# Kernel tuning notes

Measured on AMD Instinct MI355X. Metric: run time of the kernel, lower is better.

The kernel has to match this reference:

```python
import jax, jax.numpy as jnp
import numpy as np

B, N, CT, CS, CP, H, NB = 1, 1024, 768, 384, 16, 16, 4
DH = CT // H
NL, NK = 8, 32          # n_local_tokens, n_keys
K = NL + NK
SCALE = 1.0 / np.sqrt(DH)


def _ln(x, g=None, b=None, eps=1e-5):
    m = jnp.mean(x, -1, keepdims=True)
    v = jnp.var(x, -1, keepdims=True)
    y = (x - m) * jax.lax.rsqrt(v + eps)
    if g is not None:
        y = y * g
    if b is not None:
        y = y + b
    return y


def _adaln(a, s, sln_g, sw, sb, shw):
    # AF3 AdaLN: a <- sigmoid(Lin(s_n)) * LN(a) + LinNoBias(s_n)
    an = _ln(a)
    sn = _ln(s, sln_g)
    return jax.nn.sigmoid(sn @ sw + sb) * an + sn @ shw


def _indices(X_L):
    # n_local sequence neighbours (clamped window) + n_keys spatial nearest
    off = jnp.arange(NL) - NL // 2
    loc = jnp.clip(jnp.arange(N)[:, None] + off[None, :], 0, N - 1)  # [N,NL]
    d2 = jnp.sum((X_L[:, :, None, :] - X_L[:, None, :, :]) ** 2, -1)  # [B,N,N]
    _, nk = jax.lax.top_k(-d2, NK)                                    # [B,N,NK]
    loc = jnp.broadcast_to(loc[None], (X_L.shape[0], N, NL))
    return jnp.concatenate([loc, nk], -1)                             # [B,N,K]


def setup_inputs() -> dict:
    key = jax.random.key(0)
    ks = list(jax.random.split(key, 24))
    f32 = jnp.float32

    def rn(k, shape, s=0.02):
        return (jax.random.normal(k, shape) * s).astype(f32)

    d = {}
    d['A_I'] = jax.random.normal(ks[0], (B, N, CT), f32)
    d['S_I'] = jax.random.normal(ks[1], (B, N, CS), f32)
    d['Z_II'] = jax.random.normal(ks[2], (B, N, N, CP), f32)
    d['X_L'] = jax.random.normal(ks[3], (B, N, 3), f32) * 10.0
    d['f'] = jax.random.randint(ks[4], (B, N), 0, 4)
    # attention-pair-bias block params (stacked over NB blocks)
    d['aln1_sln_g'] = jnp.ones((NB, CS), f32)
    d['aln1_sw'] = rn(ks[5], (NB, CS, CT))
    d['aln1_sb'] = jnp.zeros((NB, CT), f32)
    d['aln1_shw'] = rn(ks[6], (NB, CS, CT))
    d['Wq'] = rn(ks[7], (NB, CT, CT))
    d['bq'] = jnp.zeros((NB, CT), f32)
    d['Wk'] = rn(ks[8], (NB, CT, CT))
    d['Wv'] = rn(ks[9], (NB, CT, CT))
    d['pair_ln_g'] = jnp.ones((NB, CP), f32)
    d['pair_ln_b'] = jnp.zeros((NB, CP), f32)
    d['Wb'] = rn(ks[10], (NB, CP, H))
    d['Wg'] = rn(ks[11], (NB, CT, CT))
    d['Wo'] = rn(ks[12], (NB, CT, CT))
    d['sg_w'] = rn(ks[13], (NB, CS, CT))
    d['sg_b'] = jnp.full((NB, CT), -2.0, f32)   # LinearBiasInit(-2.0)
    # conditioned transition block params
    d['aln2_sln_g'] = jnp.ones((NB, CS), f32)
    d['aln2_sw'] = rn(ks[14], (NB, CS, CT))
    d['aln2_sb'] = jnp.zeros((NB, CT), f32)
    d['aln2_shw'] = rn(ks[15], (NB, CS, CT))
    d['t_w1'] = rn(ks[16], (NB, CT, 2 * CT))
    d['t_w2'] = rn(ks[17], (NB, CT, 2 * CT))
    d['t_w3'] = rn(ks[18], (NB, 2 * CT, CT))
    d['tsg_w'] = rn(ks[19], (NB, CS, CT))
    d['tsg_b'] = jnp.full((NB, CT), -2.0, f32)
    return d


def reference(A_I, S_I, Z_II, X_L, f,
              aln1_sln_g, aln1_sw, aln1_sb, aln1_shw,
              Wq, bq, Wk, Wv, pair_ln_g, pair_ln_b, Wb, Wg, Wo, sg_w, sg_b,
              aln2_sln_g, aln2_sw, aln2_sb, aln2_shw,
              t_w1, t_w2, t_w3, tsg_w, tsg_b):
    idx = _indices(X_L)                       # [B,N,K] int
    bb = jnp.arange(B)[:, None, None]
    nn_ = jnp.arange(N)[None, :, None]
    zg = Z_II[bb, nn_, idx]                   # [B,N,K,CP] gathered pair reps
    A = A_I
    for i in range(NB):
        # LocalAttentionPairBias
        an = _adaln(A, S_I, aln1_sln_g[i], aln1_sw[i], aln1_sb[i], aln1_shw[i])
        q = (an @ Wq[i] + bq[i]).reshape(B, N, H, DH)
        kg = (an @ Wk[i])[bb, idx].reshape(B, N, K, H, DH)
        vg = (an @ Wv[i])[bb, idx].reshape(B, N, K, H, DH)
        bias = _ln(zg, pair_ln_g[i], pair_ln_b[i]) @ Wb[i]      # [B,N,K,H]
        sc = jnp.einsum('bnhd,bnkhd->bnhk', q, kg) * SCALE + jnp.swapaxes(bias, -1, -2)
        w = jax.nn.softmax(sc, -1)                               # [B,N,H,K]
        o = jnp.einsum('bnhk,bnkhd->bnhd', w, vg).reshape(B, N, CT)
        o = jax.nn.sigmoid(an @ Wg[i]) * o                       # per-channel gate
        o = jax.nn.sigmoid(S_I @ sg_w[i] + sg_b[i]) * (o @ Wo[i])
        A = A + o                                                # dropout=0 (eval)
        # ConditionedTransitionBlock (SwiGLU, n=2)
        an2 = _adaln(A, S_I, aln2_sln_g[i], aln2_sw[i], aln2_sb[i], aln2_shw[i])
        hb = jax.nn.silu(an2 @ t_w1[i]) * (an2 @ t_w2[i])
        A = A + jax.nn.sigmoid(S_I @ tsg_w[i] + tsg_b[i]) * (hb @ t_w3[i])
    return A
```

## Files before the change

kernel.cpp:

```cpp
#include <hip/hip_runtime.h>
#include <hip/hip_bf16.h>
#include <math.h>
#include <stdint.h>

#define NTOK 1024
#define CT   768
#define CS   384
#define CP   16
#define NH   16
#define DH   48
#define NBLK 4
#define NL   8
#define NKEY 32
#define KTOT 40
#define SCALE_ 0.14433756729740643f

#define WS_BLK      8257536
#define OFF_A1SW    0
#define OFF_A1SHW   294912
#define OFF_QKVG    589824
#define OFF_WO      2949120
#define OFF_SGT     3538944
#define OFF_A2SW    4128768
#define OFF_A2SHW   4423680
#define OFF_TW1     4718592
#define OFF_TW2     5898240
#define OFF_TW3     7077888

typedef __attribute__((ext_vector_type(8))) short short8;
typedef __attribute__((ext_vector_type(4))) float f32x4;

#define AS1 __attribute__((address_space(1)))
#define AS3 __attribute__((address_space(3)))

__device__ __forceinline__ float sigmoidf_(float x) {
    return 1.0f / (1.0f + __expf(-x));
}
__device__ __forceinline__ float bf2f(unsigned short u) {
    union { unsigned int i; float f; } v; v.i = (unsigned int)u << 16; return v.f;
}

__device__ __forceinline__ void gl_lds16(const void* g, void* l) {
    __builtin_amdgcn_global_load_lds((const AS1 void*)(uintptr_t)g,
                                     (AS3 void*)(uintptr_t)l, 16, 0, 0);
}

__global__ __launch_bounds__(256)
void topk_kernel(const float* __restrict__ X, int* __restrict__ idx) {
    const int w = threadIdx.x >> 6;
    const int l = threadIdx.x & 63;
    const int n = blockIdx.x * 4 + w;

    const float x0 = X[n * 3 + 0], x1 = X[n * 3 + 1], x2 = X[n * 3 + 2];
    float d[16];
    unsigned long long lkey = ~0ull;
#pragma unroll
    for (int j = 0; j < 16; ++j) {
        int m = j * 64 + l;
        float dx = x0 - X[m * 3 + 0];
        float dy = x1 - X[m * 3 + 1];
        float dz = x2 - X[m * 3 + 2];
        float v = dx * dx + dy * dy + dz * dz;
        d[j] = v;
        unsigned long long key =
            ((unsigned long long)__float_as_uint(v) << 32) | (unsigned int)m;
        lkey = key < lkey ? key : lkey;
    }
    if (l < NL) {
        int loc = n + l - NL / 2;
        loc = loc < 0 ? 0 : (loc > NTOK - 1 ? NTOK - 1 : loc);
        idx[n * KTOT + l] = loc;
    }

    for (int it = 0; it < NKEY; ++it) {
        unsigned long long rk = lkey;
#pragma unroll
        for (int s = 32; s > 0; s >>= 1) {
            unsigned long long o = __shfl_xor(rk, s, 64);
            rk = o < rk ? o : rk;
        }
        unsigned int win = (unsigned int)rk;
        if (l == 0) idx[n * KTOT + NL + it] = (int)win;
        if ((int)(win & 63) == l) {
            int jw = (int)(win >> 6);
            unsigned long long nk = ~0ull;
#pragma unroll
            for (int j = 0; j < 16; ++j) {
                if (j == jw) d[j] = INFINITY;
                unsigned long long key =
                    ((unsigned long long)__float_as_uint(d[j]) << 32) |
                    (unsigned int)(j * 64 + l);
                nk = key < nk ? key : nk;
            }
            lkey = nk;
        }
    }
}

__global__ __launch_bounds__(384)
void sprep_kernel(const float* __restrict__ S, const float* __restrict__ g1,
                  const float* __restrict__ g2,
                  __hip_bfloat16* __restrict__ S_bf,
                  __hip_bfloat16* __restrict__ snb) {
    int r = blockIdx.x, t = threadIdx.x;
    int wid = t >> 6, l = t & 63;
    __shared__ float ls[12];
    float v = S[r * CS + t];
    float s = v;
#pragma unroll
    for (int m = 32; m > 0; m >>= 1) s += __shfl_xor(s, m, 64);
    if (l == 0) ls[wid] = s;
    __syncthreads();
    float mean = (ls[0] + ls[1] + ls[2] + ls[3] + ls[4] + ls[5]) * (1.0f / CS);
    float d = v - mean;
    float q = d * d;
#pragma unroll
    for (int m = 32; m > 0; m >>= 1) q += __shfl_xor(q, m, 64);
    if (l == 0) ls[6 + wid] = q;
    __syncthreads();
    float rstd = rsqrtf((ls[6] + ls[7] + ls[8] + ls[9] + ls[10] + ls[11]) *
                        (1.0f / CS) + 1e-5f);
    float ln = d * rstd;
    S_bf[r * CS + t] = __float2bfloat16(v);
#pragma unroll
    for (int j = 0; j < 8; ++j) {
        const float* g = ((j & 1) ? g2 : g1) + (j >> 1) * CS;
        snb[((size_t)j * NTOK + r) * CS + t] = __float2bfloat16(ln * g[t]);
    }
}

__global__ __launch_bounds__(256)
void adaapply_kernel(const float* __restrict__ A,
                     const __hip_bfloat16* __restrict__ SIG,
                     const __hip_bfloat16* __restrict__ SH,
                     __hip_bfloat16* __restrict__ an) {
    int r = blockIdx.x, t = threadIdx.x;
    int wid = t >> 6, l = t & 63;
    __shared__ float ls[8];
    const float* ar = A + (size_t)r * CT;
    float v0 = ar[t], v1 = ar[t + 256], v2 = ar[t + 512];
    float s = v0 + v1 + v2;
#pragma unroll
    for (int m = 32; m > 0; m >>= 1) s += __shfl_xor(s, m, 64);
    if (l == 0) ls[wid] = s;
    __syncthreads();
    float mean = (ls[0] + ls[1] + ls[2] + ls[3]) * (1.0f / CT);
    float d0 = v0 - mean, d1 = v1 - mean, d2 = v2 - mean;
    float q = d0 * d0 + d1 * d1 + d2 * d2;
#pragma unroll
    for (int m = 32; m > 0; m >>= 1) q += __shfl_xor(q, m, 64);
    if (l == 0) ls[4 + wid] = q;
    __syncthreads();
    float rstd = rsqrtf((ls[4] + ls[5] + ls[6] + ls[7]) * (1.0f / CT) + 1e-5f);
    size_t base = (size_t)r * CT;
    float dd[3] = {d0, d1, d2};
#pragma unroll
    for (int k = 0; k < 3; ++k) {
        int c = t + k * 256;
        float sg = sigmoidf_(__bfloat162float(SIG[base + c]));
        float sh = __bfloat162float(SH[base + c]);
        an[base + c] = __float2bfloat16(sg * dd[k] * rstd + sh);
    }
}

struct ConvDesc { const float* src; __hip_bfloat16* dst; int K; int N; int tstart; int srcStride; };
struct ConvTable { ConvDesc e[14]; };

__global__ __launch_bounds__(256)
void convT_kernel(ConvTable tab) {
    int b = blockIdx.x;
    int ei = 0;
#pragma unroll
    for (int j = 1; j < 14; ++j) if (b >= tab.e[j].tstart) ei = j;
    ConvDesc d = tab.e[ei];
    const float* src = d.src + (size_t)blockIdx.y * d.srcStride;
    __hip_bfloat16* dst = d.dst + (size_t)blockIdx.y * WS_BLK;
    int tt = b - d.tstart;
    int ntn = d.N / 32;
    int k0 = (tt / ntn) * 32, n0 = (tt % ntn) * 32;
    __shared__ float s[32][33];
    int tx = threadIdx.x & 31, ty = threadIdx.x >> 5;
#pragma unroll
    for (int i = 0; i < 4; ++i)
        s[ty + 8 * i][tx] = src[(size_t)(k0 + ty + 8 * i) * d.N + n0 + tx];
    __syncthreads();
#pragma unroll
    for (int i = 0; i < 4; ++i)
        dst[(size_t)(n0 + ty + 8 * i) * d.K + k0 + tx] = __float2bfloat16(s[tx][ty + 8 * i]);
}

__global__ __launch_bounds__(256)
void biasprep_kernel(const float* __restrict__ bq, const float* __restrict__ sg_b,
                     const float* __restrict__ tsg_b, float* __restrict__ qb,
                     float* __restrict__ sb2) {
    int t = blockIdx.x * 256 + threadIdx.x;
    if (t < NBLK * 3072) {
        int i = t / 3072, c = t % 3072;
        qb[t] = (c < 768) ? bq[i * 768 + c] : 0.0f;
    }
    if (t < NBLK * 1536) {
        int i = t / 1536, c = t % 1536;
        sb2[t] = (c < 768) ? sg_b[i * 768 + c] : tsg_b[i * 768 + c - 768];
    }
}

template <int MODE>
__global__ __launch_bounds__(256)
void gemm_kernel(const __hip_bfloat16* __restrict__ A,
                 const __hip_bfloat16* B1,
                 const __hip_bfloat16* B2,
                 const float* __restrict__ cb1,
                 const float* __restrict__ cb2,
                 const __hip_bfloat16* __restrict__ auxb, int ld_aux,
                 float* __restrict__ outf,
                 __hip_bfloat16* outb,
                 __hip_bfloat16* outb2,
                 int K, int N, int ldo) {
    constexpr bool DUAL = (MODE == 2 || MODE == 5);
    __shared__ __align__(16) char As[8192];
    __shared__ __align__(16) char Bs[8192];
    __shared__ __align__(16) char Bs2[DUAL ? 8192 : 16];

    const float* cb = cb1;
    if constexpr (MODE == 5) {
        size_t z = blockIdx.z;
        A += z * (size_t)(NTOK * CS);
        B1 += (z >> 1) * (size_t)WS_BLK + (z & 1) * (size_t)OFF_A2SW;
        B2 = B1 + OFF_A1SHW;
        cb = ((z & 1) ? cb2 : cb1) + (z >> 1) * CT;
        outb += z * (size_t)(NTOK * CT);
        outb2 += z * (size_t)(NTOK * CT);
    } else if constexpr (MODE == 6) {
        size_t z = blockIdx.z;
        B1 += z * (size_t)WS_BLK;
        cb = cb1 + z * 1536;
        outb += z * (size_t)(NTOK * 1536);
    }

    const int tid = threadIdx.x;
    const int lane = tid & 63;
    const int wid = tid >> 6;
    const int wr = wid >> 1, wc = wid & 1;
    const int row0 = blockIdx.y * 64;
    const int col0 = blockIdx.x * 64;

    const int srow = tid >> 3;
    const int sg_e = (((tid & 7) ^ (srow & 7)) << 3);
    const __hip_bfloat16* ag = A + (size_t)(row0 + srow) * K + sg_e;
    const __hip_bfloat16* bg = B1 + (size_t)(col0 + srow) * K + sg_e;
    const __hip_bfloat16* bg2 = DUAL ? (B2 + (size_t)(col0 + srow) * K + sg_e) : nullptr;
    const size_t r32K = (size_t)32 * K;
    char* alds = As + tid * 16;
    char* blds = Bs + tid * 16;
    char* blds2 = Bs2 + tid * 16;

    f32x4 acc[2][2];
    f32x4 acc2[2][2];
#pragma unroll
    for (int i = 0; i < 2; ++i)
#pragma unroll
        for (int j = 0; j < 2; ++j) {
            acc[i][j] = (f32x4){0.f, 0.f, 0.f, 0.f};
            acc2[i][j] = (f32x4){0.f, 0.f, 0.f, 0.f};
        }

    const int l15 = lane & 15;
    const int lhi = lane >> 4;

    for (int k0 = 0; k0 < K; k0 += 64) {
        gl_lds16(ag, alds); gl_lds16(ag + r32K, alds + 4096);
        gl_lds16(bg, blds); gl_lds16(bg + r32K, blds + 4096);
        if (DUAL) { gl_lds16(bg2, blds2); gl_lds16(bg2 + r32K, blds2 + 4096); }
        ag += 64; bg += 64; if (DUAL) bg2 += 64;
        __syncthreads();
#pragma unroll
        for (int kk = 0; kk < 2; ++kk) {
            const int c = lhi + 4 * kk;
            const int ra0 = wr * 32 + l15, ra1 = ra0 + 16;
            const int rb0 = wc * 32 + l15, rb1 = rb0 + 16;
            short8 a0 = *(const short8*)(As + ra0 * 128 + (((c ^ (ra0 & 7)) << 4)));
            short8 a1 = *(const short8*)(As + ra1 * 128 + (((c ^ (ra1 & 7)) << 4)));
            short8 b0 = *(const short8*)(Bs + rb0 * 128 + (((c ^ (rb0 & 7)) << 4)));
            short8 b1 = *(const short8*)(Bs + rb1 * 128 + (((c ^ (rb1 & 7)) << 4)));
            acc[0][0] = __builtin_amdgcn_mfma_f32_16x16x32_bf16(a0, b0, acc[0][0], 0, 0, 0);
            acc[0][1] = __builtin_amdgcn_mfma_f32_16x16x32_bf16(a0, b1, acc[0][1], 0, 0, 0);
            acc[1][0] = __builtin_amdgcn_mfma_f32_16x16x32_bf16(a1, b0, acc[1][0], 0, 0, 0);
            acc[1][1] = __builtin_amdgcn_mfma_f32_16x16x32_bf16(a1, b1, acc[1][1], 0, 0, 0);
            if (DUAL) {
                short8 c0 = *(const short8*)(Bs2 + rb0 * 128 + (((c ^ (rb0 & 7)) << 4)));
                short8 c1 = *(const short8*)(Bs2 + rb1 * 128 + (((c ^ (rb1 & 7)) << 4)));
                acc2[0][0] = __builtin_amdgcn_mfma_f32_16x16x32_bf16(a0, c0, acc2[0][0], 0, 0, 0);
                acc2[0][1] = __builtin_amdgcn_mfma_f32_16x16x32_bf16(a0, c1, acc2[0][1], 0, 0, 0);
                acc2[1][0] = __builtin_amdgcn_mfma_f32_16x16x32_bf16(a1, c0, acc2[1][0], 0, 0, 0);
                acc2[1][1] = __builtin_amdgcn_mfma_f32_16x16x32_bf16(a1, c1, acc2[1][1], 0, 0, 0);
            }
        }
        __syncthreads();
    }

#pragma unroll
    for (int mi = 0; mi < 2; ++mi)
#pragma unroll
        for (int ni = 0; ni < 2; ++ni) {
            f32x4 v1 = acc[mi][ni];
            f32x4 v2 = acc2[mi][ni];
            int col = col0 + wc * 32 + ni * 16 + l15;
            int rbase = row0 + wr * 32 + mi * 16 + lhi * 4;
#pragma unroll
            for (int r = 0; r < 4; ++r) {
                int row = rbase + r;
                size_t o = (size_t)row * ldo + col;
                if (MODE == 2) {
                    float x = v1[r];
                    outb[o] = __float2bfloat16(x * sigmoidf_(x) * v2[r]);
                } else if (MODE == 3) {
                    float g = sigmoidf_(__bfloat162float(auxb[(size_t)row * ld_aux + col]));
                    outf[o] += g * v1[r];
                } else if (MODE == 4 || MODE == 6) {
                    outb[o] = __float2bfloat16(v1[r] + cb[col]);
                } else {
                    outb[o] = __float2bfloat16(v1[r] + cb[col]);
                    outb2[o] = __float2bfloat16(v2[r]);
                }
            }
        }
}

__global__ __launch_bounds__(256)
void attn_kernel(const __hip_bfloat16* __restrict__ qkvg,
                 const float* __restrict__ Z,
                 const int* __restrict__ idx,
                 const float* __restrict__ pg, const float* __restrict__ pb,
                 const float* __restrict__ Wbp,
                 __hip_bfloat16* __restrict__ o2) {
    int n = blockIdx.x;
    int t = threadIdx.x;
    __shared__ __align__(16) unsigned short qs[768];
    __shared__ float sc[16][48];
    __shared__ float lnz[KTOT][16];
    __shared__ float wb[16][17];
    __shared__ float pgs[16], pbs[16];
    __shared__ int sidx[KTOT];

    wb[t >> 4][t & 15] = Wbp[t];
    if (t < 96) ((short8*)qs)[t] = ((const short8*)(qkvg + (size_t)n * 3072))[t];
    if (t >= 96 && t < 96 + KTOT) sidx[t - 96] = idx[n * KTOT + (t - 96)];
    if (t >= 160 && t < 176) pgs[t - 160] = pg[t - 160];
    if (t >= 176 && t < 192) pbs[t - 176] = pb[t - 176];
    __syncthreads();

    if (t < KTOT) {
        const f32x4* z = (const f32x4*)(Z + ((size_t)n * NTOK + sidx[t]) * CP);
        f32x4 z0 = z[0], z1 = z[1], z2 = z[2], z3 = z[3];
        float v[16];
#pragma unroll
        for (int e = 0; e < 4; ++e) { v[e] = z0[e]; v[4 + e] = z1[e]; v[8 + e] = z2[e]; v[12 + e] = z3[e]; }
        float s = 0.0f;
#pragma unroll
        for (int c = 0; c < 16; ++c) s += v[c];
        float mean = s * (1.0f / 16.0f);
        float s2 = 0.0f;
#pragma unroll
        for (int c = 0; c < 16; ++c) { float d = v[c] - mean; s2 += d * d; }
        float rstd = rsqrtf(s2 * (1.0f / 16.0f) + 1e-5f);
#pragma unroll
        for (int c = 0; c < 16; ++c) lnz[t][c] = (v[c] - mean) * rstd * pgs[c] + pbs[c];
    }
    __syncthreads();

    for (int task = t; task < NH * KTOT; task += 256) {
        int h = task / KTOT, k = task - h * KTOT;
        const short8* kp = (const short8*)((const unsigned short*)qkvg +
                                           (size_t)sidx[k] * 3072 + 768 + h * DH);
        const short8* qp = (const short8*)(qs + h * DH);
        float s = 0.0f;
#pragma unroll
        for (int j = 0; j < 6; ++j) {
            short8 kv = kp[j];
            short8 qv = qp[j];
#pragma unroll
            for (int e = 0; e < 8; ++e)
                s += bf2f((unsigned short)qv[e]) * bf2f((unsigned short)kv[e]);
        }
        float bias = 0.0f;
#pragma unroll
        for (int c = 0; c < 16; ++c) bias += lnz[k][c] * wb[c][h];
        sc[h][k] = s * SCALE_ + bias;
    }
    __syncthreads();

    {
        int h = t >> 4, l = t & 15;
        float v0 = sc[h][l];
        float v1 = sc[h][l + 16];
        float v2 = (l < 8) ? sc[h][l + 32] : -INFINITY;
        float mx = fmaxf(fmaxf(v0, v1), v2);
#pragma unroll
        for (int m = 8; m > 0; m >>= 1) mx = fmaxf(mx, __shfl_xor(mx, m, 16));
        float e0 = __expf(v0 - mx), e1 = __expf(v1 - mx);
        float e2 = (l < 8) ? __expf(v2 - mx) : 0.0f;
        float sm = e0 + e1 + e2;
#pragma unroll
        for (int m = 8; m > 0; m >>= 1) sm += __shfl_xor(sm, m, 16);
        float inv = 1.0f / sm;
        sc[h][l] = e0 * inv;
        sc[h][l + 16] = e1 * inv;
        if (l < 8) sc[h][l + 32] = e2 * inv;
    }
    __syncthreads();

    if (t < 96) {
        int h = t / 6, c6 = t - h * 6;
        int d0 = c6 * 8;
        const unsigned short* vbase = (const unsigned short*)qkvg + 1536 + h * DH + d0;
        float acc[8] = {0, 0, 0, 0, 0, 0, 0, 0};
        for (int k = 0; k < KTOT; ++k) {
            short8 vv = *(const short8*)(vbase + (size_t)sidx[k] * 3072);
            float w = sc[h][k];
#pragma unroll
            for (int e = 0; e < 8; ++e) acc[e] += w * bf2f((unsigned short)vv[e]);
        }
        short8 gv = *(const short8*)((const unsigned short*)qkvg +
                                     (size_t)n * 3072 + 2304 + h * DH + d0);
        short8 ov;
#pragma unroll
        for (int e = 0; e < 8; ++e) {
            float g = sigmoidf_(bf2f((unsigned short)gv[e]));
            ov[e] = (short)__bfloat16_as_ushort(__float2bfloat16(g * acc[e]));
        }
        *(short8*)((unsigned short*)o2 + (size_t)n * CT + h * DH + d0) = ov;
    }
}

extern "C" void kernel_launch(void* const* d_in, const int* in_sizes, int n_in,
                              void* d_out, int out_size, void* d_ws, size_t ws_size,
                              hipStream_t stream) {
    const float* A_I  = (const float*)d_in[0];
    const float* S_I  = (const float*)d_in[1];
    const float* Z_II = (const float*)d_in[2];
    const float* X_L  = (const float*)d_in[3];
    const float* aln1_sln_g = (const float*)d_in[5];
    const float* aln1_sw    = (const float*)d_in[6];
    const float* aln1_sb    = (const float*)d_in[7];
    const float* aln1_shw   = (const float*)d_in[8];
    const float* Wq  = (const float*)d_in[9];
    const float* bq  = (const float*)d_in[10];
    const float* Wk  = (const float*)d_in[11];
    const float* Wv  = (const float*)d_in[12];
    const float* pair_ln_g = (const float*)d_in[13];
    const float* pair_ln_b = (const float*)d_in[14];
    const float* Wbp = (const float*)d_in[15];
    const float* Wg  = (const float*)d_in[16];
    const float* Wo  = (const float*)d_in[17];
    const float* sg_w = (const float*)d_in[18];
    const float* sg_b = (const float*)d_in[19];
    const float* aln2_sln_g = (const float*)d_in[20];
    const float* aln2_sw    = (const float*)d_in[21];
    const float* aln2_sb    = (const float*)d_in[22];
    const float* aln2_shw   = (const float*)d_in[23];
    const float* t_w1 = (const float*)d_in[24];
    const float* t_w2 = (const float*)d_in[25];
    const float* t_w3 = (const float*)d_in[26];
    const float* tsg_w = (const float*)d_in[27];
    const float* tsg_b = (const float*)d_in[28];
    (void)in_sizes; (void)n_in; (void)out_size; (void)ws_size;

    float* A = (float*)d_out;

    char* ws = (char*)d_ws;
    size_t off = 0;
    auto alloc = [&](size_t bytes) {
        void* p = ws + off;
        off += (bytes + 255) & ~(size_t)255;
        return p;
    };
    int*   idx    = (int*)  alloc(NTOK * KTOT * 4);
    __hip_bfloat16* S_bf  = (__hip_bfloat16*)alloc((size_t)NTOK * CS * 2);
    __hip_bfloat16* snb   = (__hip_bfloat16*)alloc((size_t)8 * NTOK * CS * 2);
    __hip_bfloat16* an    = (__hip_bfloat16*)alloc((size_t)NTOK * CT * 2);
    __hip_bfloat16* qkvg  = (__hip_bfloat16*)alloc((size_t)NTOK * 3072 * 2);
    __hip_bfloat16* sgateb= (__hip_bfloat16*)alloc((size_t)NBLK * NTOK * 1536 * 2);
    __hip_bfloat16* SIG   = (__hip_bfloat16*)alloc((size_t)8 * NTOK * CT * 2);
    __hip_bfloat16* SH    = (__hip_bfloat16*)alloc((size_t)8 * NTOK * CT * 2);
    __hip_bfloat16* o2    = (__hip_bfloat16*)alloc((size_t)NTOK * CT * 2);
    __hip_bfloat16* hb    = (__hip_bfloat16*)alloc((size_t)NTOK * 2 * CT * 2);
    float* qkvgbias = (float*)alloc((size_t)NBLK * 3072 * 4);
    float* sgbias   = (float*)alloc((size_t)NBLK * 1536 * 4);
    __hip_bfloat16* Wbuf = (__hip_bfloat16*)alloc((size_t)NBLK * WS_BLK * 2);

    hipMemcpyAsync(A, A_I, (size_t)NTOK * CT * 4, hipMemcpyDeviceToDevice, stream);

    topk_kernel<<<NTOK / 4, 256, 0, stream>>>(X_L, idx);
    sprep_kernel<<<NTOK, 384, 0, stream>>>(S_I, aln1_sln_g, aln2_sln_g, S_bf, snb);
    biasprep_kernel<<<NBLK * 3072 / 256, 256, 0, stream>>>(bq, sg_b, tsg_b, qkvgbias, sgbias);

    {
        ConvTable tab;
        int p = 0, ts = 0;
        auto add = [&](const float* s, size_t dstOff, int Kk, int Nn, int sstride) {
            tab.e[p].src = s; tab.e[p].dst = Wbuf + dstOff; tab.e[p].K = Kk;
            tab.e[p].N = Nn; tab.e[p].tstart = ts; tab.e[p].srcStride = sstride;
            ts += (Kk / 32) * (Nn / 32); ++p;
        };
        add(aln1_sw,  OFF_A1SW,           384, 768,  CS * CT);
        add(aln1_shw, OFF_A1SHW,          384, 768,  CS * CT);
        add(Wq, OFF_QKVG + 0 * 589824,    768, 768,  CT * CT);
        add(Wk, OFF_QKVG + 1 * 589824,    768, 768,  CT * CT);
        add(Wv, OFF_QKVG + 2 * 589824,    768, 768,  CT * CT);
        add(Wg, OFF_QKVG + 3 * 589824,    768, 768,  CT * CT);
        add(Wo, OFF_WO,                   768, 768,  CT * CT);
        add(sg_w,  OFF_SGT,               384, 768,  CS * CT);
        add(tsg_w, OFF_SGT + 768 * 384,   384, 768,  CS * CT);
        add(aln2_sw,  OFF_A2SW,           384, 768,  CS * CT);
        add(aln2_shw, OFF_A2SHW,          384, 768,  CS * CT);
        add(t_w1, OFF_TW1,                768, 1536, CT * 2 * CT);
        add(t_w2, OFF_TW2,                768, 1536, CT * 2 * CT);
        add(t_w3, OFF_TW3,                1536, 768, 2 * CT * CT);
        convT_kernel<<<dim3(ts, NBLK), 256, 0, stream>>>(tab);
    }

    gemm_kernel<5><<<dim3(12, 16, 8), 256, 0, stream>>>(
        snb, Wbuf, nullptr, aln1_sb, aln2_sb, nullptr, 0,
        nullptr, SIG, SH, 384, 768, 768);
    gemm_kernel<6><<<dim3(24, 16, 4), 256, 0, stream>>>(
        S_bf, Wbuf + OFF_SGT, nullptr, sgbias, nullptr, nullptr, 0,
        nullptr, sgateb, nullptr, 384, 1536, 1536);

    for (int i = 0; i < NBLK; ++i) {
        const __hip_bfloat16* Wb_i = Wbuf + (size_t)i * WS_BLK;
        __hip_bfloat16* sg_i = sgateb + (size_t)i * NTOK * 1536;

        adaapply_kernel<<<NTOK, 256, 0, stream>>>(
            A, SIG + (size_t)(2 * i) * NTOK * CT, SH + (size_t)(2 * i) * NTOK * CT, an);
        gemm_kernel<4><<<dim3(48, 16), 256, 0, stream>>>(
            an, Wb_i + OFF_QKVG, nullptr, qkvgbias + (size_t)i * 3072, nullptr,
            nullptr, 0, nullptr, qkvg, nullptr, 768, 3072, 3072);
        attn_kernel<<<NTOK, 256, 0, stream>>>(
            qkvg, Z_II, idx, pair_ln_g + (size_t)i * CP, pair_ln_b + (size_t)i * CP,
            Wbp + (size_t)i * CP * NH, o2);
        gemm_kernel<3><<<dim3(12, 16), 256, 0, stream>>>(
            o2, Wb_i + OFF_WO, nullptr, nullptr, nullptr, sg_i, 1536,
            A, nullptr, nullptr, 768, 768, 768);

        adaapply_kernel<<<NTOK, 256, 0, stream>>>(
            A, SIG + (size_t)(2 * i + 1) * NTOK * CT, SH + (size_t)(2 * i + 1) * NTOK * CT, an);
        gemm_kernel<2><<<dim3(24, 16), 256, 0, stream>>>(
            an, Wb_i + OFF_TW1, Wb_i + OFF_TW2, nullptr, nullptr, nullptr, 0,
            nullptr, hb, nullptr, 768, 1536, 1536);
        gemm_kernel<3><<<dim3(12, 16), 256, 0, stream>>>(
            hb, Wb_i + OFF_TW3, nullptr, nullptr, nullptr, sg_i + 768, 1536,
            A, nullptr, nullptr, 1536, 768, 768);
    }
}
```

Before: 448.0 us.

## Add 128x128-tile GEMM for large projections and vectorize weight transpose

Adds a 128x128 output-tile bf16 MFMA GEMM, each wave computing a 4x4 grid of 16x16 fragments, and uses it for the QKVG projection and the precomputed AdaLN and sigmoid-gate GEMMs. The AdaLN dual-output GEMM is split into two single-output launches over a larger z grid. The weight transpose/convert kernel moves to 64x64 tiles with vectorized float4 loads and 16-byte bf16 stores. The larger tiles cut operand reloads per FLOP but give fewer blocks (e.g. 192 for QKVG) and drop the XOR swizzle on LDS, which risks bank conflicts and lower occupancy.

```diff
diff --git a/kernel.cpp b/kernel.cpp
--- a/kernel.cpp
+++ b/kernel.cpp
@@ -39,6 +39,9 @@
 __device__ __forceinline__ float bf2f(unsigned short u) {
     union { unsigned int i; float f; } v; v.i = (unsigned int)u << 16; return v.f;
 }
+__device__ __forceinline__ unsigned short f2bf(float f) {
+    return __bfloat16_as_ushort(__float2bfloat16(f));
+}
 
 __device__ __forceinline__ void gl_lds16(const void* g, void* l) {
     __builtin_amdgcn_global_load_lds((const AS1 void*)(uintptr_t)g,
@@ -174,19 +177,33 @@
     for (int j = 1; j < 14; ++j) if (b >= tab.e[j].tstart) ei = j;
     ConvDesc d = tab.e[ei];
     const float* src = d.src + (size_t)blockIdx.y * d.srcStride;
-    __hip_bfloat16* dst = d.dst + (size_t)blockIdx.y * WS_BLK;
+    unsigned short* dst = (unsigned short*)(d.dst + (size_t)blockIdx.y * WS_BLK);
     int tt = b - d.tstart;
-    int ntn = d.N / 32;
-    int k0 = (tt / ntn) * 32, n0 = (tt % ntn) * 32;
-    __shared__ float s[32][33];
-    int tx = threadIdx.x & 31, ty = threadIdx.x >> 5;
-#pragma unroll
-    for (int i = 0; i < 4; ++i)
-        s[ty + 8 * i][tx] = src[(size_t)(k0 + ty + 8 * i) * d.N + n0 + tx];
-    __syncthreads();
-#pragma unroll
-    for (int i = 0; i < 4; ++i)
-        dst[(size_t)(n0 + ty + 8 * i) * d.K + k0 + tx] = __float2bfloat16(s[tx][ty + 8 * i]);
+    int ntn = d.N / 64;
+    int k0 = (tt / ntn) * 64, n0 = (tt % ntn) * 64;
+
+    __shared__ unsigned short lb[64 * 66];
+    const int t = threadIdx.x;
+    const int kr = t >> 4;
+    const int c4 = (t & 15) * 4;
+#pragma unroll
+    for (int it = 0; it < 4; ++it) {
+        int k = kr + it * 16;
+        f32x4 v = *(const f32x4*)&src[(size_t)(k0 + k) * d.N + n0 + c4];
+        unsigned short* p = &lb[k * 66 + c4];
+        p[0] = f2bf(v[0]); p[1] = f2bf(v[1]); p[2] = f2bf(v[2]); p[3] = f2bf(v[3]);
+    }
+    __syncthreads();
+#pragma unroll
+    for (int it = 0; it < 2; ++it) {
+        int task = t + it * 256;
+        int n = task >> 3;
+        int kc = (task & 7) * 8;
+        short8 o;
+#pragma unroll
+        for (int j = 0; j < 8; ++j) o[j] = (short)lb[(kc + j) * 66 + n];
+        *(short8*)&dst[(size_t)(n0 + n) * d.K + k0 + kc] = o;
+    }
 }
 
 __global__ __launch_bounds__(256)
@@ -206,36 +223,103 @@
 
 template <int MODE>
 __global__ __launch_bounds__(256)
-void gemm_kernel(const __hip_bfloat16* __restrict__ A,
-                 const __hip_bfloat16* B1,
-                 const __hip_bfloat16* B2,
-                 const float* __restrict__ cb1,
-                 const float* __restrict__ cb2,
-                 const __hip_bfloat16* __restrict__ auxb, int ld_aux,
-                 float* __restrict__ outf,
-                 __hip_bfloat16* outb,
-                 __hip_bfloat16* outb2,
-                 int K, int N, int ldo) {
-    constexpr bool DUAL = (MODE == 2 || MODE == 5);
+void gemm128_kernel(const __hip_bfloat16* A, const __hip_bfloat16* B1,
+                    const float* cb1, const float* cb2,
+                    __hip_bfloat16* outb, __hip_bfloat16* outb2,
+                    int K, int N, int ldo) {
+    __shared__ __align__(16) char As[8192];
+    __shared__ __align__(16) char Bs[8192];
+
+    const float* cb = cb1;
+    __hip_bfloat16* outp = outb;
+    if constexpr (MODE == 1) {
+        int z = blockIdx.z;
+        int j = z & 7, half = z >> 3;
+        A += (size_t)j * NTOK * CS;
+        B1 += (size_t)(j >> 1) * WS_BLK + ((j & 1) ? OFF_A2SW : OFF_A1SW)
+            + (size_t)half * (OFF_A1SHW - OFF_A1SW);
+        cb = half ? nullptr : (((j & 1) ? cb2 : cb1) + (j >> 1) * CT);
+        outp = (half ? outb2 : outb) + (size_t)j * NTOK * CT;
+    } else if constexpr (MODE == 2) {
+        int z = blockIdx.z;
+        B1 += (size_t)z * WS_BLK;
+        cb = cb1 + z * 1536;
+        outp = outb + (size_t)z * NTOK * 1536;
+    }
+
+    const int tid = threadIdx.x;
+    const int lane = tid & 63;
+    const int wid = tid >> 6;
+    const int wr = wid >> 1, wc = wid & 1;
+    const int row0 = blockIdx.y * 128;
+    const int col0 = blockIdx.x * 128;
+
+    const int srow = tid >> 2;
+    const int sel = (tid & 3) * 8;
+    const __hip_bfloat16* ag = A + (size_t)(row0 + srow) * K + sel;
+    const __hip_bfloat16* ag2 = A + (size_t)(row0 + 64 + srow) * K + sel;
+    const __hip_bfloat16* bg = B1 + (size_t)(col0 + srow) * K + sel;
+    const __hip_bfloat16* bg2 = B1 + (size_t)(col0 + 64 + srow) * K + sel;
+
+    f32x4 acc[4][4];
+#pragma unroll
+    for (int i = 0; i < 4; ++i)
+#pragma unroll
+        for (int j = 0; j < 4; ++j) acc[i][j] = (f32x4){0.f, 0.f, 0.f, 0.f};
+
+    const int l15 = lane & 15;
+    const int lhi = lane >> 4;
+
+    for (int k0 = 0; k0 < K; k0 += 32) {
+        gl_lds16(ag, As + tid * 16);
+        gl_lds16(ag2, As + 4096 + tid * 16);
+        gl_lds16(bg, Bs + tid * 16);
+        gl_lds16(bg2, Bs + 4096 + tid * 16);
+        ag += 32; ag2 += 32; bg += 32; bg2 += 32;
+        __syncthreads();
+        short8 a[4], b[4];
+#pragma unroll
+        for (int mi = 0; mi < 4; ++mi)
+            a[mi] = *(const short8*)(As + (wr * 64 + mi * 16 + l15) * 64 + lhi * 16);
+#pragma unroll
+        for (int ni = 0; ni < 4; ++ni)
+            b[ni] = *(const short8*)(Bs + (wc * 64 + ni * 16 + l15) * 64 + lhi * 16);
+#pragma unroll
+        for (int mi = 0; mi < 4; ++mi)
+#pragma unroll
+            for (int ni = 0; ni < 4; ++ni)
+                acc[mi][ni] = __builtin_amdgcn_mfma_f32_16x16x32_bf16(
+                    a[mi], b[ni], acc[mi][ni], 0, 0, 0);
+        __syncthreads();
+    }
+
+#pragma unroll
+    for (int mi = 0; mi < 4; ++mi)
+#pragma unroll
+        for (int ni = 0; ni < 4; ++ni) {
+            int col = col0 + wc * 64 + ni * 16 + l15;
+            int rbase = row0 + wr * 64 + mi * 16 + lhi * 4;
+            float cbv = cb ? cb[col] : 0.0f;
+            f32x4 v = acc[mi][ni];
+#pragma unroll
+            for (int r = 0; r < 4; ++r)
+                outp[(size_t)(rbase + r) * ldo + col] = __float2bfloat16(v[r] + cbv);
+        }
+}
+
+template <int MODE>
+__global__ __launch_bounds__(256)
+void gemm64_kernel(const __hip_bfloat16* __restrict__ A,
+                   const __hip_bfloat16* B1,
+                   const __hip_bfloat16* B2,
+                   const __hip_bfloat16* __restrict__ auxb, int ld_aux,
+                   float* __restrict__ outf,
+                   __hip_bfloat16* outb,
+                   int K, int N, int ldo) {
+    constexpr bool DUAL = (MODE == 2);
     __shared__ __align__(16) char As[8192];
     __shared__ __align__(16) char Bs[8192];
     __shared__ __align__(16) char Bs2[DUAL ? 8192 : 16];
-
-    const float* cb = cb1;
-    if constexpr (MODE == 5) {
-        size_t z = blockIdx.z;
-        A += z * (size_t)(NTOK * CS);
-        B1 += (z >> 1) * (size_t)WS_BLK + (z & 1) * (size_t)OFF_A2SW;
-        B2 = B1 + OFF_A1SHW;
-        cb = ((z & 1) ? cb2 : cb1) + (z >> 1) * CT;
-        outb += z * (size_t)(NTOK * CT);
-        outb2 += z * (size_t)(NTOK * CT);
-    } else if constexpr (MODE == 6) {
-        size_t z = blockIdx.z;
-        B1 += z * (size_t)WS_BLK;
-        cb = cb1 + z * 1536;
-        outb += z * (size_t)(NTOK * 1536);
-    }
 
     const int tid = threadIdx.x;
     const int lane = tid & 63;
@@ -313,14 +397,9 @@
                 if (MODE == 2) {
                     float x = v1[r];
                     outb[o] = __float2bfloat16(x * sigmoidf_(x) * v2[r]);
-                } else if (MODE == 3) {
+                } else {
                     float g = sigmoidf_(__bfloat162float(auxb[(size_t)row * ld_aux + col]));
                     outf[o] += g * v1[r];
-                } else if (MODE == 4 || MODE == 6) {
-                    outb[o] = __float2bfloat16(v1[r] + cb[col]);
-                } else {
-                    outb[o] = __float2bfloat16(v1[r] + cb[col]);
-                    outb2[o] = __float2bfloat16(v2[r]);
                 }
             }
         }
@@ -426,7 +505,7 @@
 #pragma unroll
         for (int e = 0; e < 8; ++e) {
             float g = sigmoidf_(bf2f((unsigned short)gv[e]));
-            ov[e] = (short)__bfloat16_as_ushort(__float2bfloat16(g * acc[e]));
+            ov[e] = (short)f2bf(g * acc[e]);
         }
         *(short8*)((unsigned short*)o2 + (size_t)n * CT + h * DH + d0) = ov;
     }
@@ -500,7 +579,7 @@
         auto add = [&](const float* s, size_t dstOff, int Kk, int Nn, int sstride) {
             tab.e[p].src = s; tab.e[p].dst = Wbuf + dstOff; tab.e[p].K = Kk;
             tab.e[p].N = Nn; tab.e[p].tstart = ts; tab.e[p].srcStride = sstride;
-            ts += (Kk / 32) * (Nn / 32); ++p;
+            ts += (Kk / 64) * (Nn / 64); ++p;
         };
         add(aln1_sw,  OFF_A1SW,           384, 768,  CS * CT);
         add(aln1_shw, OFF_A1SHW,          384, 768,  CS * CT);
@@ -519,12 +598,10 @@
         convT_kernel<<<dim3(ts, NBLK), 256, 0, stream>>>(tab);
     }
 
-    gemm_kernel<5><<<dim3(12, 16, 8), 256, 0, stream>>>(
-        snb, Wbuf, nullptr, aln1_sb, aln2_sb, nullptr, 0,
-        nullptr, SIG, SH, 384, 768, 768);
-    gemm_kernel<6><<<dim3(24, 16, 4), 256, 0, stream>>>(
-        S_bf, Wbuf + OFF_SGT, nullptr, sgbias, nullptr, nullptr, 0,
-        nullptr, sgateb, nullptr, 384, 1536, 1536);
+    gemm128_kernel<1><<<dim3(6, 8, 16), 256, 0, stream>>>(
+        snb, Wbuf, aln1_sb, aln2_sb, SIG, SH, 384, 768, 768);
+    gemm128_kernel<2><<<dim3(12, 8, 4), 256, 0, stream>>>(
+        S_bf, Wbuf + OFF_SGT, sgbias, nullptr, sgateb, nullptr, 384, 1536, 1536);
 
     for (int i = 0; i < NBLK; ++i) {
         const __hip_bfloat16* Wb_i = Wbuf + (size_t)i * WS_BLK;
@@ -532,23 +609,20 @@
 
         adaapply_kernel<<<NTOK, 256, 0, stream>>>(
             A, SIG + (size_t)(2 * i) * NTOK * CT, SH + (size_t)(2 * i) * NTOK * CT, an);
-        gemm_kernel<4><<<dim3(48, 16), 256, 0, stream>>>(
-            an, Wb_i + OFF_QKVG, nullptr, qkvgbias + (size_t)i * 3072, nullptr,
-            nullptr, 0, nullptr, qkvg, nullptr, 768, 3072, 3072);
+        gemm128_kernel<0><<<dim3(24, 8), 256, 0, stream>>>(
+            an, Wb_i + OFF_QKVG, qkvgbias + (size_t)i * 3072, nullptr,
+            qkvg, nullptr, 768, 3072, 3072);
         attn_kernel<<<NTOK, 256, 0, stream>>>(
             qkvg, Z_II, idx, pair_ln_g + (size_t)i * CP, pair_ln_b + (size_t)i * CP,
             Wbp + (size_t)i * CP * NH, o2);
-        gemm_kernel<3><<<dim3(12, 16), 256, 0, stream>>>(
-            o2, Wb_i + OFF_WO, nullptr, nullptr, nullptr, sg_i, 1536,
-            A, nullptr, nullptr, 768, 768, 768);
+        gemm64_kernel<3><<<dim3(12, 16), 256, 0, stream>>>(
+            o2, Wb_i + OFF_WO, nullptr, sg_i, 1536, A, nullptr, 768, 768, 768);
 
         adaapply_kernel<<<NTOK, 256, 0, stream>>>(
             A, SIG + (size_t)(2 * i + 1) * NTOK * CT, SH + (size_t)(2 * i + 1) * NTOK * CT, an);
-        gemm_kernel<2><<<dim3(24, 16), 256, 0, stream>>>(
-            an, Wb_i + OFF_TW1, Wb_i + OFF_TW2, nullptr, nullptr, nullptr, 0,
-            nullptr, hb, nullptr, 768, 1536, 1536);
-        gemm_kernel<3><<<dim3(12, 16), 256, 0, stream>>>(
-            hb, Wb_i + OFF_TW3, nullptr, nullptr, nullptr, sg_i + 768, 1536,
-            A, nullptr, nullptr, 1536, 768, 768);
-    }
-}
+        gemm64_kernel<2><<<dim3(24, 16), 256, 0, stream>>>(
+            an, Wb_i + OFF_TW1, Wb_i + OFF_TW2, nullptr, 0, nullptr, hb, 768, 1536, 1536);
+        gemm64_kernel<3><<<dim3(12, 16), 256, 0, stream>>>(
+            hb, Wb_i + OFF_TW3, nullptr, sg_i + 768, 1536, A, nullptr, 1536, 768, 768);
+    }
+}
```

Result: slower. 493.2 us (+10.1%).
